# Optimization experiments

Measured on AMD Instinct MI355X. Metric: run time of the kernel, lower is better.

Reference implementation:

```python
import jax, jax.numpy as jnp
import numpy as np

N = 50000      # nodes
E = 800000     # edges
IN = 16        # node_features_size
OUT = 32       # conv out channels
HID = 25       # edge-MLP hidden
C = 10         # num_classes


def setup_inputs() -> dict:
    key = jax.random.key(0)
    ks = jax.random.split(key, 12)
    inp = {
        "x": jax.random.normal(ks[0], (N, IN), dtype=jnp.float32),
        "edge_attr": jax.random.uniform(ks[1], (E, 1), dtype=jnp.float32),
        "edge_index": jax.random.randint(ks[2], (2, E), 0, N, dtype=jnp.int64),
        # edge-MLP nn1: Linear(1,25) -> ReLU -> Linear(25, IN*OUT)
        "w1": jax.random.normal(ks[3], (1, HID), dtype=jnp.float32) * (1.0 / np.sqrt(1)),
        "b1": jnp.zeros((HID,), dtype=jnp.float32),
        "w2": jax.random.normal(ks[4], (HID, IN * OUT), dtype=jnp.float32) * (1.0 / np.sqrt(HID)),
        "b2": jnp.zeros((IN * OUT,), dtype=jnp.float32),
        # NNConv root weight and bias
        "root": jax.random.normal(ks[5], (IN, OUT), dtype=jnp.float32) * (1.0 / np.sqrt(IN)),
        "bias": jnp.zeros((OUT,), dtype=jnp.float32),
        # fc1: Linear(32, C)
        "fc_w": jax.random.normal(ks[6], (OUT, C), dtype=jnp.float32) * (1.0 / np.sqrt(OUT)),
        "fc_b": jnp.zeros((C,), dtype=jnp.float32),
    }
    return inp


def reference(x, edge_attr, edge_index, w1, b1, w2, b2, root, bias, fc_w, fc_b):
    src = edge_index[0]  # message sources (x_j)
    dst = edge_index[1]  # aggregation targets (x_i)
    # edge MLP -> per-edge weight matrices [E, IN, OUT]
    h = jax.nn.relu(edge_attr @ w1 + b1)
    w_e = (h @ w2 + b2).reshape(-1, IN, OUT)
    # gather source features, per-edge matmul
    msg = jnp.einsum('ei,eio->eo', x[src], w_e)  # [E, OUT]
    # scatter-max aggregation to destination nodes
    agg = jax.ops.segment_max(msg, dst, num_segments=N)
    agg = jnp.where(jnp.isfinite(agg), agg, 0.0)  # empty segments -> 0
    # root transform + bias, then ELU and classifier
    out = jax.nn.elu(agg + x @ root + bias)
    logits = out @ fc_w + fc_b
    return jax.nn.log_softmax(logits, axis=1)
```

## Files before the change

### kernel.cpp

```cpp
#include <hip/hip_runtime.h>
#include <hip/hip_bf16.h>
#include <stdint.h>

#define NN   50000
#define NE   800000
#define INF_ 16
#define OUTF 32
#define HIDN 25
#define NC   10
#define QG   2048
#define QPB  16
#define DPB  32
#define NB   1563
#define EPB  8192
#define NBLK 98
#define ASTR 33
#define ECAP 2048

#define SENT 0x007FFFFFu

#define GB_PREP 128
#define GB_HIST NBLK
#define GB_XH   1563

typedef _Float16 f16x2 __attribute__((ext_vector_type(2)));

__device__ __forceinline__ uint32_t map_f(float f) {
    uint32_t b = __float_as_uint(f);
    return (b & 0x80000000u) ? ~b : (b | 0x80000000u);
}
__device__ __forceinline__ float unmap_f(uint32_t u) {
    return (u & 0x80000000u) ? __uint_as_float(u ^ 0x80000000u)
                             : __uint_as_float(~u);
}

__device__ __forceinline__ float dot2f(uint32_t g, uint32_t xb, float acc) {
#if __has_builtin(__builtin_amdgcn_fdot2)
    union { uint32_t u; f16x2 h; } ug, ux;
    ug.u = g; ux.u = xb;
    return __builtin_amdgcn_fdot2(ug.h, ux.h, acc, false);
#else
    union { uint32_t u; _Float16 h[2]; } ug, ux;
    ug.u = g; ux.u = xb;
    return fmaf((float)ug.h[0], (float)ux.h[0],
                fmaf((float)ug.h[1], (float)ux.h[1], acc));
#endif
}

__global__ __launch_bounds__(256) void prep_k(const float* __restrict__ w1,
                                              const float* __restrict__ b1,
                                              const float* __restrict__ w2,
                                              const float* __restrict__ b2,
                                              const float* __restrict__ x,
                                              const int* __restrict__ ei,
                                              uint32_t* __restrict__ G2,
                                              uint32_t* __restrict__ xh,
                                              uint32_t* __restrict__ H) {
    __shared__ union {
        struct { float w2s[HIDN * 512]; float b2s[512]; float hs[QPB][HIDN]; } g;
        uint32_t hloc[NB];
    } sm;

    const int b = blockIdx.x;
    if (b < GB_PREP) {
        for (int i = threadIdx.x; i < HIDN * 512; i += 256) sm.g.w2s[i] = w2[i];
        for (int i = threadIdx.x; i < 512; i += 256) sm.g.b2s[i] = b2[i];
        for (int i = threadIdx.x; i < QPB * HIDN; i += 256) {
            int qq = i / HIDN, k = i - qq * HIDN;
            float aq = (b * QPB + qq + 0.5f) * (1.0f / (float)QG);
            sm.g.hs[qq][k] = fmaxf(fmaf(aq, w1[k], b1[k]), 0.f);
        }
        __syncthreads();
        for (int qq = 0; qq < QPB; ++qq) {
            const int q = b * QPB + qq;
            int e = threadIdx.x;
            int ip = e >> 5, o = e & 31;
            float g0 = sm.g.b2s[(2 * ip) * OUTF + o];
            float g1 = sm.g.b2s[(2 * ip + 1) * OUTF + o];
#pragma unroll
            for (int k = 0; k < HIDN; ++k) {
                float h = sm.g.hs[qq][k];
                g0 = fmaf(h, sm.g.w2s[k * 512 + (2 * ip) * OUTF + o], g0);
                g1 = fmaf(h, sm.g.w2s[k * 512 + (2 * ip + 1) * OUTF + o], g1);
            }
            union { uint32_t u; f16x2 h2; } p;
            p.h2[0] = (_Float16)g0;
            p.h2[1] = (_Float16)g1;
            G2[(size_t)q * 256 + e] = p.u;
        }
    } else if (b < GB_PREP + GB_HIST) {
        const int blk = b - GB_PREP;
        for (int i = threadIdx.x; i < NB; i += 256) sm.hloc[i] = 0;
        __syncthreads();
        const int base = blk * EPB;
        for (int j = 0; j < EPB; j += 256) {
            int e = base + j + threadIdx.x;
            if (e < NE) atomicAdd(&sm.hloc[ei[NE + e] / DPB], 1u);
        }
        __syncthreads();
        for (int i = threadIdx.x; i < NB; i += 256)
            H[(size_t)i * NBLK + blk] = sm.hloc[i];
    } else {
        int t = (b - GB_PREP - GB_HIST) * 256 + threadIdx.x;
        if (t < NN * INF_ / 2) {
            float2 v = reinterpret_cast<const float2*>(x)[t];
            union { uint32_t u; f16x2 h; } p;
            p.h[0] = (_Float16)v.x;
            p.h[1] = (_Float16)v.y;
            xh[t] = p.u;
        }
    }
}

__global__ __launch_bounds__(256) void colsum_k(const uint32_t* __restrict__ H,
                                                uint32_t* __restrict__ Bp,
                                                uint32_t* __restrict__ tot) {
    const int bin  = (blockIdx.x * 256 + threadIdx.x) >> 6;
    const int lane = threadIdx.x & 63;
    if (bin >= NB) return;
    const uint32_t* hr = H + (size_t)bin * NBLK;
    uint32_t* br = Bp + (size_t)bin * NBLK;
    uint32_t carry = 0;
    for (int b0 = 0; b0 < NBLK; b0 += 64) {
        int b = b0 + lane;
        uint32_t v = (b < NBLK) ? hr[b] : 0;
        uint32_t inc = v;
#pragma unroll
        for (int off = 1; off < 64; off <<= 1) {
            uint32_t t = __shfl_up(inc, off);
            if (lane >= off) inc += t;
        }
        if (b < NBLK) br[b] = carry + inc - v;
        carry += __shfl(inc, 63);
    }
    if (lane == 0) tot[bin] = carry;
}

#define SCH 7
__global__ __launch_bounds__(256) void binscan_k(const uint32_t* __restrict__ tot,
                                                 uint32_t* __restrict__ bstart) {
    __shared__ uint32_t part[256];
    const int t = threadIdx.x;
    uint32_t loc[SCH];
    uint32_t s = 0;
#pragma unroll
    for (int j = 0; j < SCH; ++j) {
        int idx = t * SCH + j;
        uint32_t v = (idx < NB) ? tot[idx] : 0;
        loc[j] = s;
        s += v;
    }
    part[t] = s;
    __syncthreads();
    for (int off = 1; off < 256; off <<= 1) {
        uint32_t add = (t >= off) ? part[t - off] : 0;
        __syncthreads();
        part[t] += add;
        __syncthreads();
    }
    uint32_t base = (t > 0) ? part[t - 1] : 0;
#pragma unroll
    for (int j = 0; j < SCH; ++j) {
        int idx = t * SCH + j;
        if (idx < NB) bstart[idx] = base + loc[j];
    }
    if (t == 255) bstart[NB] = part[255];
}

__global__ __launch_bounds__(256) void scatter_k(const int* __restrict__ ei,
                                                 const float* __restrict__ ea,
                                                 const uint32_t* __restrict__ Bp,
                                                 const uint32_t* __restrict__ bstart,
                                                 uint32_t* __restrict__ sorted) {
    __shared__ uint32_t cur[NB];
    for (int i = threadIdx.x; i < NB; i += 256) cur[i] = 0;
    __syncthreads();
    const int base = blockIdx.x * EPB;
    for (int j = 0; j < EPB; j += 256) {
        int e = base + j + threadIdx.x;
        if (e < NE) {
            int s = ei[e];
            int d = ei[NE + e];
            float a = ea[e];
            int q = (int)(a * (float)QG);
            q = q < 0 ? 0 : (q > QG - 1 ? QG - 1 : q);
            int bin = d / DPB;
            uint32_t r = atomicAdd(&cur[bin], 1u);
            uint32_t pos = bstart[bin] + Bp[(size_t)bin * NBLK + blockIdx.x] + r;
            sorted[pos] = ((uint32_t)q << 21) | ((uint32_t)s << 5)
                        | (uint32_t)(d & (DPB - 1));
        }
    }
}

__global__ __launch_bounds__(256) void fused_k(const uint32_t* __restrict__ sorted,
                                               const uint32_t* __restrict__ bstart,
                                               const float* __restrict__ x,
                                               const uint32_t* __restrict__ xh,
                                               const uint32_t* __restrict__ G2,
                                               const float* __restrict__ root,
                                               const float* __restrict__ bias,
                                               const float* __restrict__ fcw,
                                               const float* __restrict__ fcb,
                                               float* __restrict__ out) {
    __shared__ uint32_t ebuf[ECAP];
    __shared__ uint32_t agg[DPB * ASTR];
    __shared__ float rs[INF_ * OUTF];
    __shared__ float bs[OUTF];
    __shared__ float fws[OUTF * NC];
    __shared__ float fbs[NC];

    const int bin  = blockIdx.x;
    const int segs = (int)bstart[bin];
    const int cnt  = (int)bstart[bin + 1] - segs;
    const int scnt = cnt < ECAP ? cnt : ECAP;

    for (int i = threadIdx.x; i < scnt; i += 256) ebuf[i] = sorted[segs + i];
    for (int i = threadIdx.x; i < DPB * ASTR; i += 256) agg[i] = SENT;
    for (int i = threadIdx.x; i < INF_ * OUTF; i += 256) rs[i] = root[i];
    if (threadIdx.x < OUTF) bs[threadIdx.x] = bias[threadIdx.x];
    for (int i = threadIdx.x; i < OUTF * NC; i += 256) fws[i] = fcw[i];
    if (threadIdx.x < NC) fbs[threadIdx.x] = fcb[threadIdx.x];
    __syncthreads();

    const int c   = threadIdx.x & 7;
    const int grp = threadIdx.x >> 3;

#define EDGE_LOAD(rec, hx0, hx1, gq)                                            \
    int db_ = (rec) & 31;                                                       \
    int src_ = ((rec) >> 5) & 0xFFFF;                                           \
    int q_ = (rec) >> 21;                                                       \
    const uint4* xp_ = reinterpret_cast<const uint4*>(xh) + src_ * 2;           \
    hx0 = xp_[0]; hx1 = xp_[1];                                                 \
    gq = reinterpret_cast<const uint4*>(G2) + (size_t)q_ * 64 + c;

#define EDGE_DOT(hx0, hx1, gq, p0, p1, p2, p3)                                  \
    {                                                                           \
        uint4 g0 = gq[0],  g1 = gq[8],  g2 = gq[16], g3 = gq[24];               \
        uint4 g4 = gq[32], g5 = gq[40], g6 = gq[48], g7 = gq[56];               \
        p0 = dot2f(g0.x, hx0.x, p0); p1 = dot2f(g0.y, hx0.x, p1);               \
        p2 = dot2f(g0.z, hx0.x, p2); p3 = dot2f(g0.w, hx0.x, p3);               \
        p0 = dot2f(g1.x, hx0.y, p0); p1 = dot2f(g1.y, hx0.y, p1);               \
        p2 = dot2f(g1.z, hx0.y, p2); p3 = dot2f(g1.w, hx0.y, p3);               \
        p0 = dot2f(g2.x, hx0.z, p0); p1 = dot2f(g2.y, hx0.z, p1);               \
        p2 = dot2f(g2.z, hx0.z, p2); p3 = dot2f(g2.w, hx0.z, p3);               \
        p0 = dot2f(g3.x, hx0.w, p0); p1 = dot2f(g3.y, hx0.w, p1);               \
        p2 = dot2f(g3.z, hx0.w, p2); p3 = dot2f(g3.w, hx0.w, p3);               \
        p0 = dot2f(g4.x, hx1.x, p0); p1 = dot2f(g4.y, hx1.x, p1);               \
        p2 = dot2f(g4.z, hx1.x, p2); p3 = dot2f(g4.w, hx1.x, p3);               \
        p0 = dot2f(g5.x, hx1.y, p0); p1 = dot2f(g5.y, hx1.y, p1);               \
        p2 = dot2f(g5.z, hx1.y, p2); p3 = dot2f(g5.w, hx1.y, p3);               \
        p0 = dot2f(g6.x, hx1.z, p0); p1 = dot2f(g6.y, hx1.z, p1);               \
        p2 = dot2f(g6.z, hx1.z, p2); p3 = dot2f(g6.w, hx1.z, p3);               \
        p0 = dot2f(g7.x, hx1.w, p0); p1 = dot2f(g7.y, hx1.w, p1);               \
        p2 = dot2f(g7.z, hx1.w, p2); p3 = dot2f(g7.w, hx1.w, p3);               \
    }

    int it = grp;
    for (; it + 32 < cnt; it += 64) {
        uint32_t recA = (it < ECAP) ? ebuf[it] : sorted[segs + it];
        int itB = it + 32;
        uint32_t recB = (itB < ECAP) ? ebuf[itB] : sorted[segs + itB];
        uint4 ax0, ax1, bx0, bx1;
        const uint4 *gqA, *gqB;
        { EDGE_LOAD(recA, ax0, ax1, gqA) (void)db_; }
        int dbA = recA & 31;
        { EDGE_LOAD(recB, bx0, bx1, gqB) (void)db_; }
        int dbB = recB & 31;

        float a0 = 0.f, a1 = 0.f, a2 = 0.f, a3 = 0.f;
        float b0 = 0.f, b1 = 0.f, b2 = 0.f, b3 = 0.f;
        EDGE_DOT(ax0, ax1, gqA, a0, a1, a2, a3)
        EDGE_DOT(bx0, bx1, gqB, b0, b1, b2, b3)

        uint32_t* agA = &agg[dbA * ASTR + c * 4];
        atomicMax(&agA[0], map_f(a0));
        atomicMax(&agA[1], map_f(a1));
        atomicMax(&agA[2], map_f(a2));
        atomicMax(&agA[3], map_f(a3));
        uint32_t* agB = &agg[dbB * ASTR + c * 4];
        atomicMax(&agB[0], map_f(b0));
        atomicMax(&agB[1], map_f(b1));
        atomicMax(&agB[2], map_f(b2));
        atomicMax(&agB[3], map_f(b3));
    }
    if (it < cnt) {
        uint32_t recA = (it < ECAP) ? ebuf[it] : sorted[segs + it];
        uint4 ax0, ax1;
        const uint4* gqA;
        { EDGE_LOAD(recA, ax0, ax1, gqA) (void)db_; }
        int dbA = recA & 31;
        float a0 = 0.f, a1 = 0.f, a2 = 0.f, a3 = 0.f;
        EDGE_DOT(ax0, ax1, gqA, a0, a1, a2, a3)
        uint32_t* agA = &agg[dbA * ASTR + c * 4];
        atomicMax(&agA[0], map_f(a0));
        atomicMax(&agA[1], map_f(a1));
        atomicMax(&agA[2], map_f(a2));
        atomicMax(&agA[3], map_f(a3));
    }
    __syncthreads();

    {
        const int li8 = threadIdx.x & 7;
        const int dl  = threadIdx.x >> 3;
        const int n   = bin * DPB + dl;
        if (n < NN) {
            const uint32_t* ar = &agg[dl * ASTR + li8 * 4];
            float av[4];
#pragma unroll
            for (int qq = 0; qq < 4; ++qq) {
                uint32_t u = ar[qq];
                av[qq] = (u == SENT) ? 0.f : unmap_f(u);
            }
            const float* xr = x + (size_t)n * INF_;
            float4 xa = *reinterpret_cast<const float4*>(xr);
            float4 xb = *reinterpret_cast<const float4*>(xr + 4);
            float4 xc = *reinterpret_cast<const float4*>(xr + 8);
            float4 xd = *reinterpret_cast<const float4*>(xr + 12);
            float xv[INF_] = {xa.x,xa.y,xa.z,xa.w, xb.x,xb.y,xb.z,xb.w,
                              xc.x,xc.y,xc.z,xc.w, xd.x,xd.y,xd.z,xd.w};
            float ov[4];
#pragma unroll
            for (int qq = 0; qq < 4; ++qq) {
                int oc = li8 * 4 + qq;
                float tv = av[qq] + bs[oc];
#pragma unroll
                for (int i = 0; i < INF_; ++i) tv = fmaf(xv[i], rs[i * OUTF + oc], tv);
                ov[qq] = (tv > 0.f) ? tv : expm1f(tv);
            }
            float lg[NC];
#pragma unroll
            for (int cc = 0; cc < NC; ++cc) {
                float tv = 0.f;
#pragma unroll
                for (int qq = 0; qq < 4; ++qq) tv = fmaf(ov[qq], fws[(li8 * 4 + qq) * NC + cc], tv);
                lg[cc] = tv;
            }
#pragma unroll
            for (int m = 1; m <= 4; m <<= 1) {
#pragma unroll
                for (int cc = 0; cc < NC; ++cc) lg[cc] += __shfl_xor(lg[cc], m);
            }
#pragma unroll
            for (int cc = 0; cc < NC; ++cc) lg[cc] += fbs[cc];

            float mx = lg[0];
#pragma unroll
            for (int cc = 1; cc < NC; ++cc) mx = fmaxf(mx, lg[cc]);
            float ssum = 0.f;
#pragma unroll
            for (int cc = 0; cc < NC; ++cc) ssum += expf(lg[cc] - mx);
            float lse = mx + logf(ssum);

            float* orow = out + (size_t)n * NC;
            orow[li8] = lg[li8] - lse;
            if (li8 < 2) orow[8 + li8] = lg[8 + li8] - lse;
        }
    }
}

extern "C" void kernel_launch(void* const* d_in, const int* in_sizes, int n_in,
                              void* d_out, int out_size, void* d_ws, size_t ws_size,
                              hipStream_t stream) {
    const float* x    = (const float*)d_in[0];
    const float* ea   = (const float*)d_in[1];
    const int*   ei   = (const int*)d_in[2];
    const float* w1   = (const float*)d_in[3];
    const float* b1   = (const float*)d_in[4];
    const float* w2   = (const float*)d_in[5];
    const float* b2   = (const float*)d_in[6];
    const float* root = (const float*)d_in[7];
    const float* bias = (const float*)d_in[8];
    const float* fcw  = (const float*)d_in[9];
    const float* fcb  = (const float*)d_in[10];
    float* out = (float*)d_out;

    size_t off = 0;
    auto alloc = [&](size_t bytes) {
        void* p = (char*)d_ws + off;
        off += (bytes + 255) & ~(size_t)255;
        return p;
    };
    uint32_t* G2       = (uint32_t*)alloc((size_t)QG * 256 * 4);
    uint32_t* xh       = (uint32_t*)alloc((size_t)NN * INF_ * 2);
    uint32_t* H        = (uint32_t*)alloc((size_t)NB * NBLK * 4);
    uint32_t* Bp       = (uint32_t*)alloc((size_t)NB * NBLK * 4);
    uint32_t* tot      = (uint32_t*)alloc((size_t)NB * 4);
    uint32_t* bstart   = (uint32_t*)alloc((size_t)(NB + 1) * 4);
    uint32_t* sorted   = (uint32_t*)alloc((size_t)NE * 4);

    prep_k<<<GB_PREP + GB_HIST + GB_XH, 256, 0, stream>>>(w1, b1, w2, b2, x, ei, G2, xh, H);
    colsum_k<<<(NB * 64 + 255) / 256, 256, 0, stream>>>(H, Bp, tot);
    binscan_k<<<1, 256, 0, stream>>>(tot, bstart);
    scatter_k<<<NBLK, 256, 0, stream>>>(ei, ea, Bp, bstart, sorted);
    fused_k<<<NB, 256, 0, stream>>>(sorted, bstart, x, xh, G2, root, bias, fcw, fcb, out);
}
```

Measured before the change: 93.08 us.

## Fold histogram scan into scatter kernel and halve destinations per bin

Removes the colsum and binscan kernels. Each scatter block now recomputes its own per-bin prefix and the global bin scan from a transposed histogram, which saves two launches and their global round trips at the cost of redundant work in every block. Bins shrink to 16 destinations, giving 3125 fused blocks with a smaller edge cache, and the scatter/histogram blocks double their edge count. The x-to-fp16 conversion is widened to 8 elements per thread.

```diff
diff --git a/kernel.cpp b/kernel.cpp
--- a/kernel.cpp
+++ b/kernel.cpp
@@ -10,18 +10,19 @@
 #define NC   10
 #define QG   2048
 #define QPB  16
-#define DPB  32
-#define NB   1563
-#define EPB  8192
-#define NBLK 98
+#define DPB  16
+#define NB   3125
+#define EPB  16384
+#define NBLK 49
 #define ASTR 33
-#define ECAP 2048
+#define ECAP 768
+#define SCH  13
 
 #define SENT 0x007FFFFFu
 
 #define GB_PREP 128
 #define GB_HIST NBLK
-#define GB_XH   1563
+#define GB_XH   391
 
 typedef _Float16 f16x2 __attribute__((ext_vector_type(2)));
 
@@ -95,100 +96,96 @@
         const int base = blk * EPB;
         for (int j = 0; j < EPB; j += 256) {
             int e = base + j + threadIdx.x;
-            if (e < NE) atomicAdd(&sm.hloc[ei[NE + e] / DPB], 1u);
+            if (e < NE) atomicAdd(&sm.hloc[ei[NE + e] >> 4], 1u);
         }
         __syncthreads();
         for (int i = threadIdx.x; i < NB; i += 256)
-            H[(size_t)i * NBLK + blk] = sm.hloc[i];
+            H[(size_t)blk * NB + i] = sm.hloc[i];
     } else {
-        int t = (b - GB_PREP - GB_HIST) * 256 + threadIdx.x;
-        if (t < NN * INF_ / 2) {
-            float2 v = reinterpret_cast<const float2*>(x)[t];
-            union { uint32_t u; f16x2 h; } p;
-            p.h[0] = (_Float16)v.x;
-            p.h[1] = (_Float16)v.y;
-            xh[t] = p.u;
-        }
-    }
-}
-
-__global__ __launch_bounds__(256) void colsum_k(const uint32_t* __restrict__ H,
-                                                uint32_t* __restrict__ Bp,
-                                                uint32_t* __restrict__ tot) {
-    const int bin  = (blockIdx.x * 256 + threadIdx.x) >> 6;
-    const int lane = threadIdx.x & 63;
-    if (bin >= NB) return;
-    const uint32_t* hr = H + (size_t)bin * NBLK;
-    uint32_t* br = Bp + (size_t)bin * NBLK;
-    uint32_t carry = 0;
-    for (int b0 = 0; b0 < NBLK; b0 += 64) {
-        int b = b0 + lane;
-        uint32_t v = (b < NBLK) ? hr[b] : 0;
-        uint32_t inc = v;
-#pragma unroll
-        for (int off = 1; off < 64; off <<= 1) {
-            uint32_t t = __shfl_up(inc, off);
-            if (lane >= off) inc += t;
-        }
-        if (b < NBLK) br[b] = carry + inc - v;
-        carry += __shfl(inc, 63);
-    }
-    if (lane == 0) tot[bin] = carry;
-}
-
-#define SCH 7
-__global__ __launch_bounds__(256) void binscan_k(const uint32_t* __restrict__ tot,
-                                                 uint32_t* __restrict__ bstart) {
+        int t4 = ((b - GB_PREP - GB_HIST) * 256 + threadIdx.x) * 4;
+        if (t4 < NN * INF_ / 2) {
+            const float4* xp = reinterpret_cast<const float4*>(x) + (t4 >> 1);
+            float4 va = xp[0];
+            float4 vb = xp[1];
+            union { uint32_t u[4]; f16x2 h[4]; } p;
+            p.h[0][0] = (_Float16)va.x; p.h[0][1] = (_Float16)va.y;
+            p.h[1][0] = (_Float16)va.z; p.h[1][1] = (_Float16)va.w;
+            p.h[2][0] = (_Float16)vb.x; p.h[2][1] = (_Float16)vb.y;
+            p.h[3][0] = (_Float16)vb.z; p.h[3][1] = (_Float16)vb.w;
+            *reinterpret_cast<uint4*>(xh + t4) = make_uint4(p.u[0], p.u[1], p.u[2], p.u[3]);
+        }
+    }
+}
+
+__global__ __launch_bounds__(256) void scatter_k(const int* __restrict__ ei,
+                                                 const float* __restrict__ ea,
+                                                 const uint32_t* __restrict__ H,
+                                                 uint32_t* __restrict__ bstart,
+                                                 uint32_t* __restrict__ sorted) {
+    __shared__ uint32_t cur[NB];
+    __shared__ uint32_t pref[NB];
+    __shared__ uint32_t bst[NB + 1];
     __shared__ uint32_t part[256];
-    const int t = threadIdx.x;
+    const int myblk = blockIdx.x;
+    const int tid = threadIdx.x;
+
+    for (int bin = tid; bin < NB; bin += 256) {
+        uint32_t p = 0, tt = 0;
+        for (int b = 0; b < NBLK; ++b) {
+            uint32_t v = H[(size_t)b * NB + bin];
+            tt += v;
+            if (b < myblk) p += v;
+        }
+        pref[bin] = p;
+        bst[bin] = tt;
+        cur[bin] = 0;
+    }
+    __syncthreads();
+
     uint32_t loc[SCH];
     uint32_t s = 0;
 #pragma unroll
     for (int j = 0; j < SCH; ++j) {
-        int idx = t * SCH + j;
-        uint32_t v = (idx < NB) ? tot[idx] : 0;
+        int idx = tid * SCH + j;
+        uint32_t v = (idx < NB) ? bst[idx] : 0;
         loc[j] = s;
         s += v;
     }
-    part[t] = s;
+    part[tid] = s;
     __syncthreads();
     for (int off = 1; off < 256; off <<= 1) {
-        uint32_t add = (t >= off) ? part[t - off] : 0;
-        __syncthreads();
-        part[t] += add;
-        __syncthreads();
-    }
-    uint32_t base = (t > 0) ? part[t - 1] : 0;
+        uint32_t add = (tid >= off) ? part[tid - off] : 0;
+        __syncthreads();
+        part[tid] += add;
+        __syncthreads();
+    }
+    uint32_t base = (tid > 0) ? part[tid - 1] : 0;
+    __syncthreads();
 #pragma unroll
     for (int j = 0; j < SCH; ++j) {
-        int idx = t * SCH + j;
-        if (idx < NB) bstart[idx] = base + loc[j];
-    }
-    if (t == 255) bstart[NB] = part[255];
-}
-
-__global__ __launch_bounds__(256) void scatter_k(const int* __restrict__ ei,
-                                                 const float* __restrict__ ea,
-                                                 const uint32_t* __restrict__ Bp,
-                                                 const uint32_t* __restrict__ bstart,
-                                                 uint32_t* __restrict__ sorted) {
-    __shared__ uint32_t cur[NB];
-    for (int i = threadIdx.x; i < NB; i += 256) cur[i] = 0;
-    __syncthreads();
-    const int base = blockIdx.x * EPB;
+        int idx = tid * SCH + j;
+        if (idx < NB) bst[idx] = base + loc[j];
+    }
+    if (tid == 255) bst[NB] = part[255];
+    __syncthreads();
+
+    if (myblk == 0)
+        for (int i = tid; i <= NB; i += 256) bstart[i] = bst[i];
+
+    const int ebase = myblk * EPB;
     for (int j = 0; j < EPB; j += 256) {
-        int e = base + j + threadIdx.x;
+        int e = ebase + j + tid;
         if (e < NE) {
-            int s = ei[e];
-            int d = ei[NE + e];
+            int sn = ei[e];
+            int d  = ei[NE + e];
             float a = ea[e];
             int q = (int)(a * (float)QG);
             q = q < 0 ? 0 : (q > QG - 1 ? QG - 1 : q);
-            int bin = d / DPB;
+            int bin = d >> 4;
             uint32_t r = atomicAdd(&cur[bin], 1u);
-            uint32_t pos = bstart[bin] + Bp[(size_t)bin * NBLK + blockIdx.x] + r;
-            sorted[pos] = ((uint32_t)q << 21) | ((uint32_t)s << 5)
-                        | (uint32_t)(d & (DPB - 1));
+            uint32_t pos = bst[bin] + pref[bin] + r;
+            sorted[pos] = ((uint32_t)q << 21) | ((uint32_t)sn << 5)
+                        | (uint32_t)(d & 15);
         }
     }
 }
@@ -227,7 +224,6 @@
     const int grp = threadIdx.x >> 3;
 
 #define EDGE_LOAD(rec, hx0, hx1, gq)                                            \
-    int db_ = (rec) & 31;                                                       \
     int src_ = ((rec) >> 5) & 0xFFFF;                                           \
     int q_ = (rec) >> 21;                                                       \
     const uint4* xp_ = reinterpret_cast<const uint4*>(xh) + src_ * 2;           \
@@ -263,10 +259,10 @@
         uint32_t recB = (itB < ECAP) ? ebuf[itB] : sorted[segs + itB];
         uint4 ax0, ax1, bx0, bx1;
         const uint4 *gqA, *gqB;
-        { EDGE_LOAD(recA, ax0, ax1, gqA) (void)db_; }
-        int dbA = recA & 31;
-        { EDGE_LOAD(recB, bx0, bx1, gqB) (void)db_; }
-        int dbB = recB & 31;
+        { EDGE_LOAD(recA, ax0, ax1, gqA) }
+        int dbA = recA & 15;
+        { EDGE_LOAD(recB, bx0, bx1, gqB) }
+        int dbB = recB & 15;
 
         float a0 = 0.f, a1 = 0.f, a2 = 0.f, a3 = 0.f;
         float b0 = 0.f, b1 = 0.f, b2 = 0.f, b3 = 0.f;
@@ -288,8 +284,8 @@
         uint32_t recA = (it < ECAP) ? ebuf[it] : sorted[segs + it];
         uint4 ax0, ax1;
         const uint4* gqA;
-        { EDGE_LOAD(recA, ax0, ax1, gqA) (void)db_; }
-        int dbA = recA & 31;
+        { EDGE_LOAD(recA, ax0, ax1, gqA) }
+        int dbA = recA & 15;
         float a0 = 0.f, a1 = 0.f, a2 = 0.f, a3 = 0.f;
         EDGE_DOT(ax0, ax1, gqA, a0, a1, a2, a3)
         uint32_t* agA = &agg[dbA * ASTR + c * 4];
@@ -304,7 +300,7 @@
         const int li8 = threadIdx.x & 7;
         const int dl  = threadIdx.x >> 3;
         const int n   = bin * DPB + dl;
-        if (n < NN) {
+        if (dl < DPB && n < NN) {
             const uint32_t* ar = &agg[dl * ASTR + li8 * 4];
             float av[4];
 #pragma unroll
@@ -383,15 +379,11 @@
     };
     uint32_t* G2       = (uint32_t*)alloc((size_t)QG * 256 * 4);
     uint32_t* xh       = (uint32_t*)alloc((size_t)NN * INF_ * 2);
-    uint32_t* H        = (uint32_t*)alloc((size_t)NB * NBLK * 4);
-    uint32_t* Bp       = (uint32_t*)alloc((size_t)NB * NBLK * 4);
-    uint32_t* tot      = (uint32_t*)alloc((size_t)NB * 4);
+    uint32_t* H        = (uint32_t*)alloc((size_t)NBLK * NB * 4);
     uint32_t* bstart   = (uint32_t*)alloc((size_t)(NB + 1) * 4);
     uint32_t* sorted   = (uint32_t*)alloc((size_t)NE * 4);
 
     prep_k<<<GB_PREP + GB_HIST + GB_XH, 256, 0, stream>>>(w1, b1, w2, b2, x, ei, G2, xh, H);
-    colsum_k<<<(NB * 64 + 255) / 256, 256, 0, stream>>>(H, Bp, tot);
-    binscan_k<<<1, 256, 0, stream>>>(tot, bstart);
-    scatter_k<<<NBLK, 256, 0, stream>>>(ei, ea, Bp, bstart, sorted);
+    scatter_k<<<NBLK, 256, 0, stream>>>(ei, ea, H, bstart, sorted);
     fused_k<<<NB, 256, 0, stream>>>(sorted, bstart, x, xh, G2, root, bias, fcw, fcb, out);
 }
```

Result: slower. 113.3 us (+21.7%).
